# Performance work log

Hardware: AMD Instinct MI355X
Metric: run time of the kernel (lower is better)

Reference implementation:

```python
import jax, jax.numpy as jnp
import numpy as np

N = 100_000      # nodes
E = 3_000_000    # edges
G = 256          # graphs in batch
F_IN = 64        # num_features
NHID = 32


def setup_inputs() -> dict:
    key = jax.random.key(0)
    ks = jax.random.split(key, 12)
    x = jax.random.normal(ks[0], (N, F_IN), dtype=jnp.float32)
    edge_index = jax.random.randint(ks[1], (2, E), 0, N, dtype=jnp.int32)
    batch = jnp.sort(jax.random.randint(ks[2], (N,), 0, G, dtype=jnp.int32))
    # disjoint edge partitions used as integer index arrays (as in the torch code)
    perm = jax.random.permutation(ks[3], E).astype(jnp.int32)
    third = E // 3
    known_mask = perm[:third]
    unk_mask = perm[third:2 * third]
    obs_mask = perm[2 * third:]
    msg_weights = jax.random.normal(ks[4], (3,), dtype=jnp.float32)
    emb_W = jax.random.normal(ks[5], (F_IN - 1, 63), dtype=jnp.float32) * 0.1
    emb_b = jnp.zeros((63,), jnp.float32)
    gcn_W = jax.random.normal(ks[6], (64, NHID), dtype=jnp.float32) * 0.1
    gcn_b = jnp.zeros((NHID,), jnp.float32)
    fc1_W = jax.random.normal(ks[7], (NHID, NHID), dtype=jnp.float32) * 0.1
    fc1_b = jnp.zeros((NHID,), jnp.float32)
    out_W = jax.random.normal(ks[8], (NHID, 1), dtype=jnp.float32) * 0.1
    out_b = jnp.zeros((1,), jnp.float32)
    return dict(x=x, edge_index=edge_index, batch=batch, known_mask=known_mask,
                unk_mask=unk_mask, obs_mask=obs_mask, msg_weights=msg_weights,
                emb_W=emb_W, emb_b=emb_b, gcn_W=gcn_W, gcn_b=gcn_b,
                fc1_W=fc1_W, fc1_b=fc1_b, out_W=out_W, out_b=out_b)


def reference(x, edge_index, batch, known_mask, unk_mask, obs_mask,
              msg_weights, emb_W, emb_b, gcn_W, gcn_b,
              fc1_W, fc1_b, out_W, out_b):
    n_nodes = x.shape[0]
    n_edges = edge_index.shape[1]
    # edge weights from softmaxed message-type params (disjoint index sets)
    sp = jax.nn.softmax(msg_weights)
    ew = jnp.ones((n_edges,), x.dtype)
    ew = ew.at[known_mask].set(sp[0]).at[unk_mask].set(sp[1]).at[obs_mask].set(sp[2])
    # feature embed: keep col 0, embed the remaining 63 -> 63, concat to 64
    h = jnp.concatenate([x[:, :1], x[:, 1:] @ emb_W + emb_b], axis=1)  # [N,64]
    # GCNConv: add self-loops (weight 1), symmetric normalization
    loops = jnp.arange(n_nodes, dtype=edge_index.dtype)
    row = jnp.concatenate([edge_index[0], loops])
    col = jnp.concatenate([edge_index[1], loops])
    w = jnp.concatenate([ew, jnp.ones((n_nodes,), ew.dtype)])
    deg = jax.ops.segment_sum(w, col, num_segments=n_nodes)
    dinv = jnp.where(deg > 0, jax.lax.rsqrt(deg), 0.0)
    norm = dinv[row] * w * dinv[col]                   # [E+N]
    hW = h @ gcn_W                                     # [N,nhid]
    msg = norm[:, None] * hW[row]                      # gather + scale
    agg = jax.ops.segment_sum(msg, col, num_segments=n_nodes) + gcn_b
    hg = jax.nn.relu(agg)                              # dropout = identity (eval)
    pooled = jax.ops.segment_sum(hg, batch, num_segments=G)  # global_add_pool
    z = jax.nn.relu(pooled @ fc1_W + fc1_b)
    return z @ out_W + out_b                           # [G,1]
```

## Files before the change

kernel.cpp:

```cpp
#include <hip/hip_runtime.h>
#include <hip/hip_fp16.h>
#include <stdint.h>


#define BLK 256
#define NCHUNK 512
#define CHKSH 13
#define CHK 8192
#define NCB 128
#define CELLCAP 96
#define MAXNB 1600
#define ENTCAP 2560

__global__ void kA1(const int* __restrict__ col, int* __restrict__ cnt,
                    int n_edges, int NB,
                    const int* __restrict__ km, const int* __restrict__ um,
                    int s0, int s1,
                    uint16_t* __restrict__ kl, int* __restrict__ cnt2) {
    int t = threadIdx.x;
    if (blockIdx.x < NCHUNK) {
        __shared__ int lh[MAXNB];
        int c = blockIdx.x;
        for (int b = t; b < NB; b += BLK) lh[b] = 0;
        __syncthreads();
        int e0 = c << CHKSH, e1 = min(e0 + CHK, n_edges);
        for (int e = e0 + t; e < e1; e += BLK) atomicAdd(&lh[col[e] >> 6], 1);
        __syncthreads();
        for (int b = t; b < NB; b += BLK) cnt[(size_t)c * NB + b] = lh[b];
    } else {
        __shared__ int cur2[NCHUNK];
        int b = blockIdx.x - NCHUNK;
        for (int i = t; i < NCHUNK; i += BLK) cur2[i] = 0;
        __syncthreads();
        int total = s0 + s1;
        int slice = (total + NCB - 1) / NCB;
        int i0 = b * slice, i1 = min(i0 + slice, total);
        for (int i = i0 + t; i < i1; i += BLK) {
            int e, cls;
            if (i < s0) { e = km[i];      cls = 0; }
            else        { e = um[i - s0]; cls = 1; }
            int bu = e >> CHKSH;
            int pos = atomicAdd(&cur2[bu], 1);
            if (pos < CELLCAP)
                kl[((size_t)bu * NCB + b) * CELLCAP + pos] =
                    (uint16_t)(((e & (CHK - 1)) << 1) | cls);
        }
        __syncthreads();
        for (int i = t; i < NCHUNK; i += BLK) cnt2[(size_t)b * NCHUNK + i] = cur2[i];
    }
}

__global__ void kB2(const int* __restrict__ cnt, int* __restrict__ offTT,
                    int* __restrict__ tot, int NB) {
    __shared__ int tile[NCHUNK * 16];
    __shared__ int segs[16][17];
    int t = threadIdx.x;
    int b0 = blockIdx.x * 16;
    for (int idx = t; idx < NCHUNK * 16; idx += BLK) {
        int c = idx >> 4, b = idx & 15;
        tile[idx] = (b0 + b < NB) ? cnt[(size_t)c * NB + b0 + b] : 0;
    }
    __syncthreads();
    int b = t & 15, seg = t >> 4;
    int psum = 0;
#pragma unroll
    for (int k = 0; k < 32; ++k) psum += tile[(seg * 32 + k) * 16 + b];
    segs[seg][b] = psum;
    __syncthreads();
    int ex = 0;
    for (int ss = 0; ss < seg; ++ss) ex += segs[ss][b];
    int run = ex;
#pragma unroll
    for (int k = 0; k < 32; ++k) {
        int c = seg * 32 + k;
        if (b0 + b < NB) offTT[(size_t)c * NB + b0 + b] = run;
        run += tile[c * 16 + b];
    }
    if (seg == 15 && b0 + b < NB) tot[b0 + b] = run;
}

__global__ void kBase3(const int* __restrict__ tot, int* __restrict__ base_, int NB,
                       const float* __restrict__ emb_W, const float* __restrict__ emb_b,
                       const float* __restrict__ gcn_W,
                       float* __restrict__ Wfull, float* __restrict__ hWbias) {
    int t = threadIdx.x;
    if (blockIdx.x < 8) {
        int k = blockIdx.x * 8 + (t >> 5), j = t & 31;
        float acc;
        if (k == 0) {
            acc = gcn_W[j];
        } else {
            int m = k - 1;
            acc = 0.0f;
#pragma unroll 9
            for (int tt = 0; tt < 63; ++tt)
                acc += emb_W[m * 63 + tt] * gcn_W[(1 + tt) * 32 + j];
        }
        Wfull[k * 32 + j] = acc;
        if (blockIdx.x == 0 && t < 32) {
            float bacc = 0.0f;
            for (int tt = 0; tt < 63; ++tt)
                bacc += emb_b[tt] * gcn_W[(1 + tt) * 32 + t];
            hWbias[t] = bacc;
        }
    } else {
        __shared__ int s[BLK];
        const int K = 7;
        int v[K]; int sum = 0;
#pragma unroll
        for (int k = 0; k < K; ++k) {
            int i = t * K + k;
            v[k] = (i < NB) ? tot[i] : 0;
            sum += v[k];
        }
        s[t] = sum; __syncthreads();
        for (int st = 1; st < BLK; st <<= 1) {
            int x = (t >= st) ? s[t - st] : 0;
            __syncthreads(); s[t] += x; __syncthreads();
        }
        int ex = (t == 0) ? 0 : s[t - 1];
#pragma unroll
        for (int k = 0; k < K; ++k) {
            int i = t * K + k;
            if (i < NB) base_[i] = ex;
            ex += v[k];
        }
        if (t == BLK - 1) base_[NB] = s[BLK - 1];
    }
}

__global__ void kC_scatter(const int* __restrict__ row, const int* __restrict__ col,
                           const uint16_t* __restrict__ kl, const int* __restrict__ cnt2,
                           const int* __restrict__ base_,
                           const int* __restrict__ offTT, int* __restrict__ csrB,
                           int n_edges, int NB) {
    __shared__ int cur[MAXNB];
    __shared__ uint8_t clsL[CHK];
    __shared__ int cnt2s[NCB];
    int t = threadIdx.x;
    int nused = (n_edges + CHK - 1) >> CHKSH;
    int xcd = blockIdx.x & 7, ord = blockIdx.x >> 3;
    int q = nused >> 3, r = nused & 7;
    int len = (xcd < r) ? q + 1 : q;
    if (ord >= len) return;
    int c = (xcd < r) ? xcd * (q + 1) + ord
                      : r * (q + 1) + (xcd - r) * q + ord;
    const int* offrow = offTT + (size_t)c * NB;
    for (int b = t; b < NB; b += BLK) cur[b] = base_[b] + offrow[b];
    for (int i = t; i < CHK; i += BLK) clsL[i] = 2;
    if (t < NCB) cnt2s[t] = cnt2[(size_t)t * NCHUNK + c];
    __syncthreads();
    for (int idx = t; idx < NCB * CELLCAP; idx += BLK) {
        int b2 = idx / CELLCAP, i = idx - b2 * CELLCAP;
        if (i < cnt2s[b2]) {
            uint16_t v = kl[((size_t)c * NCB + b2) * CELLCAP + i];
            clsL[v >> 1] = (uint8_t)(v & 1);
        }
    }
    __syncthreads();
    int e0 = c << CHKSH, e1 = min(e0 + CHK, n_edges);
    for (int e = e0 + t; e < e1; e += BLK) {
        int cc = col[e];
        int pos = atomicAdd(&cur[cc >> 6], 1);
        csrB[pos] = ((cc & 63) << 19) | (row[e] << 2) | clsL[e - e0];
    }
}

__global__ void k4f_gemm(const float* __restrict__ x, const float* __restrict__ Wfull,
                         const float* __restrict__ hWbias, const int* __restrict__ base_,
                         const int* __restrict__ csrB, const float* __restrict__ mw,
                         __half* __restrict__ hWs, int n_nodes) {
    __shared__ float Wl[64 * 32];
    __shared__ float xs[64 * 64];
    __shared__ int ct4[256];
    __shared__ float dv[64];
    int b = blockIdx.x, t = threadIdx.x;
    for (int idx = t; idx < 2048; idx += BLK) Wl[idx] = Wfull[idx];
    if (t < 256) ct4[t] = 0;
    int rowBase = b * 64;
    for (int idx = t; idx < 4096; idx += BLK) {
        int r = rowBase + (idx >> 6);
        xs[idx] = (r < n_nodes) ? x[(size_t)r * 64 + (idx & 63)] : 0.0f;
    }
    __syncthreads();
    int p0 = base_[b], p1 = base_[b + 1];
    for (int p = p0 + t; p < p1; p += BLK) {
        int e = csrB[p];
        atomicAdd(&ct4[((e >> 19) << 2) | (e & 3)], 1);
    }
    __syncthreads();
    if (t < 64) {
        float a = mw[0], bb = mw[1], c3 = mw[2];
        float m = fmaxf(a, fmaxf(bb, c3));
        float ea = __expf(a - m), eb = __expf(bb - m), ec = __expf(c3 - m);
        float inv = 1.0f / (ea + eb + ec);
        float deg = (ea * inv) * (float)ct4[t * 4]
                  + (eb * inv) * (float)ct4[t * 4 + 1]
                  + (ec * inv) * (float)ct4[t * 4 + 2]
                  + (float)ct4[t * 4 + 3]
                  + 1.0f;
        dv[t] = rsqrtf(deg);
    }
    __syncthreads();
    int j = t & 31, lr = t >> 5;
#pragma unroll
    for (int k8 = 0; k8 < 8; ++k8) {
        int r = lr + 8 * k8;
        int n = rowBase + r;
        if (n < n_nodes) {
            float acc = hWbias[j];
#pragma unroll
            for (int k = 0; k < 64; ++k)
                acc += xs[r * 64 + k] * Wl[k * 32 + j];
            hWs[(size_t)n * 32 + j] = __float2half(dv[r] * acc);
        }
    }
}

__global__ void kD_gather(const int* __restrict__ base_, const int* __restrict__ csrB,
                          const __half2* __restrict__ hws2,
                          const float* __restrict__ mw, const float* __restrict__ gcn_b,
                          const int* __restrict__ batch, float* __restrict__ pooled,
                          int n_nodes) {
    __shared__ int ent[ENTCAP];
    __shared__ int raw[ENTCAP];
    __shared__ float res[64 * 33];
    __shared__ int ct4[256];
    __shared__ int ct[64], st[64], cur[64];
    __shared__ float dl[64], gb[32];
    __shared__ int bl[64];
    int b = blockIdx.x, t = threadIdx.x;
    if (t < 256) ct4[t] = 0;
    if (t < 64) {
        int n = b * 64 + t;
        bl[t] = (n < n_nodes) ? batch[n] : -1;
    }
    if (t < 32) gb[t] = gcn_b[t];
    __syncthreads();
    int p0 = base_[b], p1 = base_[b + 1];
    int m = min(p1 - p0, ENTCAP);
    for (int i = t; i < m; i += BLK) {
        int e = csrB[p0 + i];
        raw[i] = e;
        atomicAdd(&ct4[((e >> 19) << 2) | (e & 3)], 1);
    }
    __syncthreads();
    float a = mw[0], bb = mw[1], c3 = mw[2];
    float mx = fmaxf(a, fmaxf(bb, c3));
    float ea = __expf(a - mx), eb = __expf(bb - mx), ec = __expf(c3 - mx);
    float inv = 1.0f / (ea + eb + ec);
    float w0 = ea * inv, w1 = eb * inv, w2 = ec * inv;
    if (t < 64) {
        int c0 = ct4[t * 4], c1 = ct4[t * 4 + 1], c2 = ct4[t * 4 + 2], c33 = ct4[t * 4 + 3];
        ct[t] = c0 + c1 + c2 + c33;
        dl[t] = rsqrtf(w0 * (float)c0 + w1 * (float)c1 + w2 * (float)c2
                       + (float)c33 + 1.0f);
    }
    __syncthreads();
    if (t < 64) st[t] = ct[t];
    __syncthreads();
    for (int off = 1; off < 64; off <<= 1) {
        int v = (t < 64 && t >= off) ? st[t - off] : 0;
        __syncthreads();
        if (t < 64) st[t] += v;
        __syncthreads();
    }
    if (t < 64) { st[t] -= ct[t]; cur[t] = st[t]; }
    __syncthreads();
    for (int i = t; i < m; i += BLK) {
        int e = raw[i];
        int pos = atomicAdd(&cur[e >> 19], 1);
        ent[pos] = e;
    }
    __syncthreads();
    int grp = t >> 4, j2 = t & 15;
#pragma unroll
    for (int idx = 0; idx < 4; ++idx) {
        int lc = grp + 16 * idx;
        int n = b * 64 + lc;
        float rx = 0.0f, ry = 0.0f;
        if (n < n_nodes) {
            int s = st[lc], end = s + ct[lc];
            float ax = 0.0f, ay = 0.0f;
            int p = s;
            for (; p + 8 <= end; p += 8) {
                int e0 = ent[p],     e1 = ent[p + 1], e2 = ent[p + 2], e3 = ent[p + 3];
                int e4 = ent[p + 4], e5 = ent[p + 5], e6 = ent[p + 6], e7 = ent[p + 7];
                __half2 h0 = hws2[(size_t)((e0 >> 2) & 0x1FFFF) * 16 + j2];
                __half2 h1 = hws2[(size_t)((e1 >> 2) & 0x1FFFF) * 16 + j2];
                __half2 h2 = hws2[(size_t)((e2 >> 2) & 0x1FFFF) * 16 + j2];
                __half2 h3 = hws2[(size_t)((e3 >> 2) & 0x1FFFF) * 16 + j2];
                __half2 h4 = hws2[(size_t)((e4 >> 2) & 0x1FFFF) * 16 + j2];
                __half2 h5 = hws2[(size_t)((e5 >> 2) & 0x1FFFF) * 16 + j2];
                __half2 h6 = hws2[(size_t)((e6 >> 2) & 0x1FFFF) * 16 + j2];
                __half2 h7 = hws2[(size_t)((e7 >> 2) & 0x1FFFF) * 16 + j2];
                float f0 = ((e0 & 3) == 0) ? w0 : (((e0 & 3) == 1) ? w1 : w2);
                float f1 = ((e1 & 3) == 0) ? w0 : (((e1 & 3) == 1) ? w1 : w2);
                float f2 = ((e2 & 3) == 0) ? w0 : (((e2 & 3) == 1) ? w1 : w2);
                float f3 = ((e3 & 3) == 0) ? w0 : (((e3 & 3) == 1) ? w1 : w2);
                float f4 = ((e4 & 3) == 0) ? w0 : (((e4 & 3) == 1) ? w1 : w2);
                float f5 = ((e5 & 3) == 0) ? w0 : (((e5 & 3) == 1) ? w1 : w2);
                float f6 = ((e6 & 3) == 0) ? w0 : (((e6 & 3) == 1) ? w1 : w2);
                float f7 = ((e7 & 3) == 0) ? w0 : (((e7 & 3) == 1) ? w1 : w2);
                float2 g0 = __half22float2(h0), g1 = __half22float2(h1);
                float2 g2 = __half22float2(h2), g3 = __half22float2(h3);
                float2 g4 = __half22float2(h4), g5 = __half22float2(h5);
                float2 g6 = __half22float2(h6), g7 = __half22float2(h7);
                ax += f0 * g0.x + f1 * g1.x + f2 * g2.x + f3 * g3.x
                    + f4 * g4.x + f5 * g5.x + f6 * g6.x + f7 * g7.x;
                ay += f0 * g0.y + f1 * g1.y + f2 * g2.y + f3 * g3.y
                    + f4 * g4.y + f5 * g5.y + f6 * g6.y + f7 * g7.y;
            }
            for (; p < end; ++p) {
                int e0 = ent[p];
                __half2 h0 = hws2[(size_t)((e0 >> 2) & 0x1FFFF) * 16 + j2];
                float f0 = ((e0 & 3) == 0) ? w0 : (((e0 & 3) == 1) ? w1 : w2);
                float2 g0 = __half22float2(h0);
                ax += f0 * g0.x; ay += f0 * g0.y;
            }
            float2 self = __half22float2(hws2[(size_t)n * 16 + j2]);
            float di = dl[lc];
            rx = fmaxf(di * (ax + self.x) + gb[2 * j2], 0.0f);
            ry = fmaxf(di * (ay + self.y) + gb[2 * j2 + 1], 0.0f);
        }
        res[lc * 33 + 2 * j2]     = rx;
        res[lc * 33 + 2 * j2 + 1] = ry;
    }
    __syncthreads();
    if (t < 32) {
        int j = t;
        float sum = 0.0f; int g0 = bl[0];
        for (int lc = 0; lc < 64; ++lc) {
            if (bl[lc] < 0) break;
            float val = res[lc * 33 + j];
            if (bl[lc] != g0) { atomicAdd(&pooled[g0 * 32 + j], sum); sum = 0.0f; g0 = bl[lc]; }
            sum += val;
        }
        if (g0 >= 0) atomicAdd(&pooled[g0 * 32 + j], sum);
    }
}

__global__ void k7_head(const float* __restrict__ pooled, const float* __restrict__ fc1_W,
                        const float* __restrict__ fc1_b, const float* __restrict__ out_W,
                        const float* __restrict__ out_b, float* __restrict__ out,
                        int n_graphs) {
    __shared__ float Wl[32 * 32];
    __shared__ float bl[32];
    __shared__ float owl[32];
    int t = threadIdx.x;
    for (int idx = t; idx < 1024; idx += BLK) Wl[idx] = fc1_W[idx];
    if (t < 32) { bl[t] = fc1_b[t]; owl[t] = out_W[t]; }
    __syncthreads();
    if (t < n_graphs) {
        float p[32];
#pragma unroll
        for (int k = 0; k < 32; ++k) p[k] = pooled[t * 32 + k];
        float acc = 0.0f;
        for (int j = 0; j < 32; ++j) {
            float z = bl[j];
#pragma unroll
            for (int k = 0; k < 32; ++k) z += p[k] * Wl[k * 32 + j];
            z = fmaxf(z, 0.0f);
            acc += z * owl[j];
        }
        out[t] = acc + out_b[0];
    }
}

static inline size_t align_up(size_t v, size_t a) { return (v + a - 1) & ~(a - 1); }

extern "C" void kernel_launch(void* const* d_in, const int* in_sizes, int n_in,
                              void* d_out, int out_size, void* d_ws, size_t ws_size,
                              hipStream_t stream) {
    const float* x     = (const float*)d_in[0];
    const int*   ei    = (const int*)d_in[1];
    const int*   batch = (const int*)d_in[2];
    const int*   km    = (const int*)d_in[3];
    const int*   um    = (const int*)d_in[4];
    const int*   om    = (const int*)d_in[5];
    const float* mw    = (const float*)d_in[6];
    const float* emb_W = (const float*)d_in[7];
    const float* emb_b = (const float*)d_in[8];
    const float* gcn_W = (const float*)d_in[9];
    const float* gcn_b = (const float*)d_in[10];
    const float* fc1_W = (const float*)d_in[11];
    const float* fc1_b = (const float*)d_in[12];
    const float* out_W = (const float*)d_in[13];
    const float* out_b = (const float*)d_in[14];
    (void)om;

    const int n_nodes  = in_sizes[0] / 64;
    const int n_edges  = in_sizes[1] / 2;
    const int s0 = in_sizes[3], s1 = in_sizes[4];
    const int n_graphs = out_size;

    const int* row = ei;
    const int* col = ei + n_edges;

    const int NB  = (n_nodes + 63) >> 6;
    const int NGB = (NB + 15) / 16;

    char* base = (char*)d_ws;
    float*   pooled = (float*)base;   base += (size_t)n_graphs * 32 * 4;
    int*     cnt    = (int*)base;     base += (size_t)NCHUNK * NB * 4;
    int*     offTT  = (int*)base;     base += (size_t)NCHUNK * NB * 4;
    int*     tot    = (int*)base;     base += (size_t)NB * 4;
    int*     base_  = (int*)base;     base += (size_t)(NB + 1) * 4;
    float*   Wfull  = (float*)base;   base += 2048 * 4;
    float*   hWbias = (float*)base;   base += 32 * 4;
    int*     cnt2   = (int*)base;     base += (size_t)NCB * NCHUNK * 4;
    int*     csrB   = (int*)base;     base += (size_t)n_edges * 4;
    base = (char*)align_up((size_t)base, 64);
    uint16_t* kl  = (uint16_t*)base;
    __half*   hWs = (__half*)base;
    base += (size_t)NCHUNK * NCB * CELLCAP * 2;

    hipMemsetAsync(pooled, 0, (size_t)n_graphs * 32 * 4, stream);

    kA1<<<NCHUNK + NCB, BLK, 0, stream>>>(col, cnt, n_edges, NB, km, um, s0, s1,
                                          kl, cnt2);
    kB2<<<NGB, BLK, 0, stream>>>(cnt, offTT, tot, NB);
    kBase3<<<9, BLK, 0, stream>>>(tot, base_, NB, emb_W, emb_b, gcn_W, Wfull, hWbias);
    kC_scatter<<<NCHUNK, BLK, 0, stream>>>(row, col, kl, cnt2, base_, offTT, csrB,
                                           n_edges, NB);
    k4f_gemm<<<NB, BLK, 0, stream>>>(x, Wfull, hWbias, base_, csrB, mw, hWs, n_nodes);
    kD_gather<<<NB, BLK, 0, stream>>>(base_, csrB, (const __half2*)hWs, mw,
                                      gcn_b, batch, pooled, n_nodes);
    k7_head<<<1, BLK, 0, stream>>>(pooled, fc1_W, fc1_b, out_W, out_b, (float*)d_out, n_graphs);
}
```

Before: 314.1 us.

## Halve edge chunk size, store per-chunk counts as uint16, drop gather staging buffer

```diff
diff --git a/kernel.cpp b/kernel.cpp
--- a/kernel.cpp
+++ b/kernel.cpp
@@ -4,15 +4,15 @@
 
 
 #define BLK 256
-#define NCHUNK 512
-#define CHKSH 13
-#define CHK 8192
+#define NCHUNK 1024
+#define CHKSH 12
+#define CHK 4096
 #define NCB 128
-#define CELLCAP 96
+#define CELLCAP 56
 #define MAXNB 1600
 #define ENTCAP 2560
 
-__global__ void kA1(const int* __restrict__ col, int* __restrict__ cnt,
+__global__ void kA1(const int* __restrict__ col, uint16_t* __restrict__ cnt,
                     int n_edges, int NB,
                     const int* __restrict__ km, const int* __restrict__ um,
                     int s0, int s1,
@@ -26,7 +26,7 @@
         int e0 = c << CHKSH, e1 = min(e0 + CHK, n_edges);
         for (int e = e0 + t; e < e1; e += BLK) atomicAdd(&lh[col[e] >> 6], 1);
         __syncthreads();
-        for (int b = t; b < NB; b += BLK) cnt[(size_t)c * NB + b] = lh[b];
+        for (int b = t; b < NB; b += BLK) cnt[(size_t)c * NB + b] = (uint16_t)lh[b];
     } else {
         __shared__ int cur2[NCHUNK];
         int b = blockIdx.x - NCHUNK;
@@ -50,31 +50,31 @@
     }
 }
 
-__global__ void kB2(const int* __restrict__ cnt, int* __restrict__ offTT,
+__global__ void kB2(const uint16_t* __restrict__ cnt, uint16_t* __restrict__ offTT,
                     int* __restrict__ tot, int NB) {
-    __shared__ int tile[NCHUNK * 16];
+    __shared__ uint16_t tile[NCHUNK * 16];
     __shared__ int segs[16][17];
     int t = threadIdx.x;
     int b0 = blockIdx.x * 16;
     for (int idx = t; idx < NCHUNK * 16; idx += BLK) {
         int c = idx >> 4, b = idx & 15;
-        tile[idx] = (b0 + b < NB) ? cnt[(size_t)c * NB + b0 + b] : 0;
+        tile[idx] = (b0 + b < NB) ? cnt[(size_t)c * NB + b0 + b] : (uint16_t)0;
     }
     __syncthreads();
     int b = t & 15, seg = t >> 4;
     int psum = 0;
 #pragma unroll
-    for (int k = 0; k < 32; ++k) psum += tile[(seg * 32 + k) * 16 + b];
+    for (int k = 0; k < 64; ++k) psum += (int)tile[(seg * 64 + k) * 16 + b];
     segs[seg][b] = psum;
     __syncthreads();
     int ex = 0;
     for (int ss = 0; ss < seg; ++ss) ex += segs[ss][b];
     int run = ex;
 #pragma unroll
-    for (int k = 0; k < 32; ++k) {
-        int c = seg * 32 + k;
-        if (b0 + b < NB) offTT[(size_t)c * NB + b0 + b] = run;
-        run += tile[c * 16 + b];
+    for (int k = 0; k < 64; ++k) {
+        int c = seg * 64 + k;
+        if (b0 + b < NB) offTT[(size_t)c * NB + b0 + b] = (uint16_t)run;
+        run += (int)tile[c * 16 + b];
     }
     if (seg == 15 && b0 + b < NB) tot[b0 + b] = run;
 }
@@ -132,7 +132,7 @@
 __global__ void kC_scatter(const int* __restrict__ row, const int* __restrict__ col,
                            const uint16_t* __restrict__ kl, const int* __restrict__ cnt2,
                            const int* __restrict__ base_,
-                           const int* __restrict__ offTT, int* __restrict__ csrB,
+                           const uint16_t* __restrict__ offTT, int* __restrict__ csrB,
                            int n_edges, int NB) {
     __shared__ int cur[MAXNB];
     __shared__ uint8_t clsL[CHK];
@@ -145,8 +145,8 @@
     if (ord >= len) return;
     int c = (xcd < r) ? xcd * (q + 1) + ord
                       : r * (q + 1) + (xcd - r) * q + ord;
-    const int* offrow = offTT + (size_t)c * NB;
-    for (int b = t; b < NB; b += BLK) cur[b] = base_[b] + offrow[b];
+    const uint16_t* offrow = offTT + (size_t)c * NB;
+    for (int b = t; b < NB; b += BLK) cur[b] = base_[b] + (int)offrow[b];
     for (int i = t; i < CHK; i += BLK) clsL[i] = 2;
     if (t < NCB) cnt2s[t] = cnt2[(size_t)t * NCHUNK + c];
     __syncthreads();
@@ -223,7 +223,6 @@
                           const int* __restrict__ batch, float* __restrict__ pooled,
                           int n_nodes) {
     __shared__ int ent[ENTCAP];
-    __shared__ int raw[ENTCAP];
     __shared__ float res[64 * 33];
     __shared__ int ct4[256];
     __shared__ int ct[64], st[64], cur[64];
@@ -239,9 +238,9 @@
     __syncthreads();
     int p0 = base_[b], p1 = base_[b + 1];
     int m = min(p1 - p0, ENTCAP);
-    for (int i = t; i < m; i += BLK) {
-        int e = csrB[p0 + i];
-        raw[i] = e;
+    int p1c = p0 + m;
+    for (int p = p0 + t; p < p1c; p += BLK) {
+        int e = csrB[p];
         atomicAdd(&ct4[((e >> 19) << 2) | (e & 3)], 1);
     }
     __syncthreads();
@@ -267,8 +266,8 @@
     }
     if (t < 64) { st[t] -= ct[t]; cur[t] = st[t]; }
     __syncthreads();
-    for (int i = t; i < m; i += BLK) {
-        int e = raw[i];
+    for (int p = p0 + t; p < p1c; p += BLK) {
+        int e = csrB[p];
         int pos = atomicAdd(&cur[e >> 19], 1);
         ent[pos] = e;
     }
@@ -401,15 +400,15 @@
     const int NGB = (NB + 15) / 16;
 
     char* base = (char*)d_ws;
-    float*   pooled = (float*)base;   base += (size_t)n_graphs * 32 * 4;
-    int*     cnt    = (int*)base;     base += (size_t)NCHUNK * NB * 4;
-    int*     offTT  = (int*)base;     base += (size_t)NCHUNK * NB * 4;
-    int*     tot    = (int*)base;     base += (size_t)NB * 4;
-    int*     base_  = (int*)base;     base += (size_t)(NB + 1) * 4;
-    float*   Wfull  = (float*)base;   base += 2048 * 4;
-    float*   hWbias = (float*)base;   base += 32 * 4;
-    int*     cnt2   = (int*)base;     base += (size_t)NCB * NCHUNK * 4;
-    int*     csrB   = (int*)base;     base += (size_t)n_edges * 4;
+    float*    pooled = (float*)base;    base += (size_t)n_graphs * 32 * 4;
+    uint16_t* cnt    = (uint16_t*)base; base += (size_t)NCHUNK * NB * 2;
+    uint16_t* offTT  = (uint16_t*)base; base += (size_t)NCHUNK * NB * 2;
+    int*      tot    = (int*)base;      base += (size_t)NB * 4;
+    int*      base_  = (int*)base;      base += (size_t)(NB + 1) * 4;
+    float*    Wfull  = (float*)base;    base += 2048 * 4;
+    float*    hWbias = (float*)base;    base += 32 * 4;
+    int*      cnt2   = (int*)base;      base += (size_t)NCB * NCHUNK * 4;
+    int*      csrB   = (int*)base;      base += (size_t)n_edges * 4;
     base = (char*)align_up((size_t)base, 64);
     uint16_t* kl  = (uint16_t*)base;
     __half*   hWs = (__half*)base;
```

After: 300.3 us. -4.4%, faster.
